# Performance work log

Measured on AMD Instinct MI355X. Metric: run time of the kernel, lower is better.

The kernel has to match this reference:

```python
import jax, jax.numpy as jnp
import numpy as np

LN_EPS = 1e-5


def setup_inputs() -> dict:
    key = jax.random.key(0)
    ks = jax.random.split(key, 10)
    N, E, D, H = 32000, 512000, 256, 128
    atom_features = jax.random.normal(ks[0], (N, D), dtype=jnp.float32)
    edge_features = jax.random.normal(ks[1], (E, H), dtype=jnp.float32)
    edge_index = jax.random.randint(ks[2], (2, E), 0, N, dtype=jnp.int64)
    s = lambda fan_in: 1.0 / np.sqrt(fan_in)
    W_lin = jax.random.normal(ks[3], (D, H), dtype=jnp.float32) * s(D)
    W1 = jax.random.normal(ks[4], (3 * H, H), dtype=jnp.float32) * s(3 * H)
    b1 = jnp.zeros((H,), jnp.float32)
    W2 = jax.random.normal(ks[5], (H, H), dtype=jnp.float32) * s(H)
    b2 = jnp.zeros((H,), jnp.float32)
    W3 = jax.random.normal(ks[6], (H, H), dtype=jnp.float32) * s(H)
    b3 = jnp.zeros((H,), jnp.float32)
    gamma = jnp.ones((H,), jnp.float32)
    beta = jnp.zeros((H,), jnp.float32)
    return dict(atom_features=atom_features, edge_features=edge_features,
                edge_index=edge_index, W_lin=W_lin, W1=W1, b1=b1, W2=W2,
                b2=b2, W3=W3, b3=b3, gamma=gamma, beta=beta)


def _layernorm(x, gamma, beta):
    mu = jnp.mean(x, axis=-1, keepdims=True)
    var = jnp.mean((x - mu) ** 2, axis=-1, keepdims=True)
    return (x - mu) * jax.lax.rsqrt(var + LN_EPS) * gamma + beta


def reference(atom_features, edge_features, edge_index, W_lin, W1, b1, W2, b2, W3, b3, gamma, beta):
    # o3.Linear on scalar irreps -> plain bias-free linear: [N, D] @ [D, H]
    atom_scalars = atom_features @ W_lin  # [N, H]
    edge_dst, edge_src = edge_index[0], edge_index[1]
    # gather + concat: [E, 3H]
    edge_in = jnp.concatenate(
        [atom_scalars[edge_dst], atom_scalars[edge_src], edge_features], axis=-1)
    h = jax.nn.relu(edge_in @ W1 + b1)
    h = jax.nn.relu(h @ W2 + b2)
    h = h @ W3 + b3  # [E, H]
    return _layernorm(edge_features + h, gamma, beta)
```

## Files before the change

### kernel.cpp

```cpp
#include <hip/hip_runtime.h>

typedef __attribute__((ext_vector_type(8))) short bf16x8;
typedef __attribute__((ext_vector_type(16))) float f32x16;
typedef __attribute__((ext_vector_type(4))) float f32x4;
typedef __attribute__((ext_vector_type(4))) unsigned u32x4;

#define LN_EPS 1e-5f

__device__ __forceinline__ unsigned short f2bf(float f) {
    unsigned u = __float_as_uint(f);
    unsigned r = (u + 0x7FFFu + ((u >> 16) & 1u)) >> 16;
    return (unsigned short)r;
}

__device__ __forceinline__ unsigned cvt_pk_bf16(float lo, float hi) {
    unsigned r;
    asm("v_cvt_pk_bf16_f32 %0, %1, %2" : "=v"(r) : "v"(lo), "v"(hi));
    return r;
}

__device__ __forceinline__ void permswap(unsigned& a, unsigned& b) {
    asm("v_permlane32_swap_b32 %0, %1" : "+v"(a), "+v"(b));
}

__global__ void prep_weights(const float* __restrict__ W_lin,
                             const float* __restrict__ W1,
                             const float* __restrict__ W2,
                             const float* __restrict__ W3,
                             unsigned short* __restrict__ wt_lin,
                             unsigned short* __restrict__ wimg) {
    int i = blockIdx.x * blockDim.x + threadIdx.x;
    if (i < 128 * 256) {
        int n = i >> 8, k = i & 255;
        wt_lin[n * 256 + k] = f2bf(W_lin[k * 128 + n]);
    } else if (i < 128 * 256 + 5 * 16384) {
        int j = i - 128 * 256;
        int mat = j >> 14, r = j & 16383;
        int jj = r & 7, l = (r >> 3) & 63, ks = (r >> 9) & 7, f = r >> 12;
        int n = 32 * f + (l & 31);
        int k = 16 * ks + 8 * (l >> 5) + jj;
        float v;
        if (mat < 3)       v = W1[(mat * 128 + k) * 128 + n];
        else if (mat == 3) v = W2[k * 128 + n];
        else               v = W3[k * 128 + n];
        wimg[j] = f2bf(v);
    }
}

__global__ void atoms_gemm(const float* __restrict__ af,
                           const unsigned short* __restrict__ wt_lin,
                           unsigned short* __restrict__ atoms_bf,
                           int Natoms) {
    const int wv = threadIdx.x >> 6, lane = threadIdx.x & 63;
    const int l31 = lane & 31, g8 = (lane >> 5) * 8, g4 = (lane >> 5) * 4;
    const int R = blockIdx.x * 128 + wv * 32;

    f32x16 acc[4];
#pragma unroll
    for (int f = 0; f < 4; ++f)
#pragma unroll
        for (int e = 0; e < 16; ++e) acc[f][e] = 0.0f;

    int arow = R + l31;
    if (arow >= Natoms) arow = Natoms - 1;
    const float* ap = af + (size_t)arow * 256;

#pragma unroll
    for (int ks = 0; ks < 16; ++ks) {
        const int k0 = ks * 16 + g8;
        float4 x0 = *(const float4*)(ap + k0);
        float4 x1 = *(const float4*)(ap + k0 + 4);
        bf16x8 a;
        a[0] = (short)f2bf(x0.x); a[1] = (short)f2bf(x0.y);
        a[2] = (short)f2bf(x0.z); a[3] = (short)f2bf(x0.w);
        a[4] = (short)f2bf(x1.x); a[5] = (short)f2bf(x1.y);
        a[6] = (short)f2bf(x1.z); a[7] = (short)f2bf(x1.w);
#pragma unroll
        for (int f = 0; f < 4; ++f) {
            bf16x8 b = *(const bf16x8*)(wt_lin + (32 * f + l31) * 256 + k0);
            acc[f] = __builtin_amdgcn_mfma_f32_32x32x16_bf16(a, b, acc[f], 0, 0, 0);
        }
    }

#pragma unroll
    for (int f = 0; f < 4; ++f) {
        const int col = 32 * f + l31;
#pragma unroll
        for (int r = 0; r < 16; ++r) {
            int row = R + (r & 3) + 8 * (r >> 2) + g4;
            if (row < Natoms) atoms_bf[(size_t)row * 128 + col] = f2bf(acc[f][r]);
        }
    }
}

__global__ __launch_bounds__(512, 2) void edge_fused(
    const float* __restrict__ ef, const int* __restrict__ eidx,
    const unsigned short* __restrict__ atoms_bf,
    const unsigned short* __restrict__ wimg,
    const float* __restrict__ b1, const float* __restrict__ b2,
    const float* __restrict__ b3, const float* __restrict__ gamma_,
    const float* __restrict__ beta_, float* __restrict__ out, int E) {
    __shared__ unsigned short wlds[2 * 16384];
    __shared__ unsigned short io[8][4096];

    const int tid = threadIdx.x;
    const int lane = tid & 63, wv = tid >> 6;
    const int l31 = lane & 31, hi = lane >> 5, h8 = hi * 8;

    {
        const char* s = (const char*)wimg;
        char* d = (char*)wlds;
        const int o = tid * 16;
#pragma unroll
        for (int i = 0; i < 8; ++i)
            __builtin_amdgcn_global_load_lds(
                (const __attribute__((address_space(1))) unsigned int*)(s + o + i * 8192),
                (__attribute__((address_space(3))) unsigned int*)(d + o + i * 8192),
                16, 0, 0);
    }

    const int edgeBase = blockIdx.x * 256 + wv * 32;
    const int e0 = edgeBase + l31;
    const int e = e0 < E ? e0 : E - 1;

    const int dI = eidx[e], sI = eidx[E + e];
    const unsigned short* dRow = atoms_bf + (size_t)dI * 128;
    const unsigned short* sRow = atoms_bf + (size_t)sI * 128;
    bf16x8 gd[8], gs[8];
#pragma unroll
    for (int ks = 0; ks < 8; ++ks) {
        gd[ks] = *(const bf16x8*)(dRow + ks * 16 + h8);
        gs[ks] = *(const bf16x8*)(sRow + ks * 16 + h8);
    }

    char* iow = (char*)&io[wv][0];
    {
        const int r4 = lane >> 4;
        const int c8 = (lane & 15) * 8;
#pragma unroll
        for (int i = 0; i < 8; ++i) {
            const int row = i * 4 + r4;
            int gr = edgeBase + row;
            if (gr >= E) gr = E - 1;
            const float* rp = ef + (size_t)gr * 128 + c8;
            f32x4 x0 = *(const f32x4*)(rp);
            f32x4 x1 = *(const f32x4*)(rp + 4);
            u32x4 w = (u32x4){cvt_pk_bf16(x0[0], x0[1]), cvt_pk_bf16(x0[2], x0[3]),
                              cvt_pk_bf16(x1[0], x1[1]), cvt_pk_bf16(x1[2], x1[3])};
            const int slot = (lane & 15) ^ (row & 7);
            *(u32x4*)(iow + row * 256 + slot * 16) = w;
        }
    }

#pragma unroll
    for (int ks = 0; ks < 8; ++ks)
        asm volatile("" :: "v"(gd[ks]), "v"(gs[ks]));

    f32x16 acc[4];
    auto initb = [&](const float* __restrict__ bb) {
#pragma unroll
        for (int f = 0; f < 4; ++f)
#pragma unroll
            for (int m = 0; m < 4; ++m) {
                f32x4 b4 = *(const f32x4*)(bb + 32 * f + 8 * m + 4 * hi);
#pragma unroll
                for (int i = 0; i < 4; ++i) acc[f][4 * m + i] = b4[i];
            }
    };

    bf16x8 frag[8];
    auto build_frags = [&]() {
#pragma unroll
        for (int f = 0; f < 4; ++f) {
            unsigned pk0[4], pk1[4];
#pragma unroll
            for (int m = 0; m < 4; ++m) {
                float a0 = fmaxf(acc[f][4 * m + 0], 0.0f);
                float a1 = fmaxf(acc[f][4 * m + 1], 0.0f);
                float a2 = fmaxf(acc[f][4 * m + 2], 0.0f);
                float a3 = fmaxf(acc[f][4 * m + 3], 0.0f);
                pk0[m] = cvt_pk_bf16(a0, a1);
                pk1[m] = cvt_pk_bf16(a2, a3);
            }
#pragma unroll
            for (int k1 = 0; k1 < 2; ++k1) {
                unsigned x0 = pk0[2 * k1], y0 = pk0[2 * k1 + 1];
                unsigned x1 = pk1[2 * k1], y1 = pk1[2 * k1 + 1];
                permswap(x0, y0);
                permswap(x1, y1);
                union { u32x4 u; bf16x8 b; } cv;
                cv.u = (u32x4){x0, x1, y0, y1};
                frag[2 * f + k1] = cv.b;
            }
        }
    };

    const unsigned short* lbase = wlds + lane * 8;
    const unsigned short* wg1c = wimg + 2 * 16384 + lane * 8;
    const unsigned short* wg2 = wimg + 3 * 16384 + lane * 8;
    const unsigned short* wg3 = wimg + 4 * 16384 + lane * 8;
    const int xr = l31 & 7;

    __syncthreads();

    initb(b1);
#pragma unroll
    for (int ks = 0; ks < 8; ++ks)
#pragma unroll
        for (int f = 0; f < 4; ++f) {
            bf16x8 a = *(const bf16x8*)(lbase + ((0 * 4 + f) * 8 + ks) * 512);
            acc[f] = __builtin_amdgcn_mfma_f32_32x32x16_bf16(a, gd[ks], acc[f], 0, 0, 0);
        }
#pragma unroll
    for (int ks = 0; ks < 8; ++ks)
#pragma unroll
        for (int f = 0; f < 4; ++f) {
            bf16x8 a = *(const bf16x8*)(lbase + ((1 * 4 + f) * 8 + ks) * 512);
            acc[f] = __builtin_amdgcn_mfma_f32_32x32x16_bf16(a, gs[ks], acc[f], 0, 0, 0);
        }
#pragma unroll
    for (int ks = 0; ks < 8; ++ks) {
        const int slot = (2 * ks + hi) ^ xr;
        bf16x8 bx = *(const bf16x8*)(iow + l31 * 256 + slot * 16);
#pragma unroll
        for (int f = 0; f < 4; ++f) {
            bf16x8 a = *(const bf16x8*)(wg1c + (f * 8 + ks) * 512);
            acc[f] = __builtin_amdgcn_mfma_f32_32x32x16_bf16(a, bx, acc[f], 0, 0, 0);
        }
    }

    build_frags();
    initb(b2);
#pragma unroll
    for (int ks = 0; ks < 8; ++ks)
#pragma unroll
        for (int f = 0; f < 4; ++f) {
            bf16x8 a = *(const bf16x8*)(wg2 + (f * 8 + ks) * 512);
            acc[f] = __builtin_amdgcn_mfma_f32_32x32x16_bf16(a, frag[ks], acc[f], 0, 0, 0);
        }

    build_frags();
    initb(b3);
#pragma unroll
    for (int ks = 0; ks < 8; ++ks)
#pragma unroll
        for (int f = 0; f < 4; ++f) {
            bf16x8 a = *(const bf16x8*)(wg3 + (f * 8 + ks) * 512);
            acc[f] = __builtin_amdgcn_mfma_f32_32x32x16_bf16(a, frag[ks], acc[f], 0, 0, 0);
        }

    float s = 0.0f, q = 0.0f;
#pragma unroll
    for (int f = 0; f < 4; ++f)
#pragma unroll
        for (int m = 0; m < 4; ++m) {
            const int slot = (4 * f + m) ^ xr;
            uint2 w = *(const uint2*)(iow + l31 * 256 + slot * 16 + 8 * hi);
            float r0 = __uint_as_float(w.x << 16);
            float r1 = __uint_as_float(w.x & 0xffff0000u);
            float r2 = __uint_as_float(w.y << 16);
            float r3 = __uint_as_float(w.y & 0xffff0000u);
            float v0 = acc[f][4 * m + 0] + r0;
            float v1 = acc[f][4 * m + 1] + r1;
            float v2 = acc[f][4 * m + 2] + r2;
            float v3 = acc[f][4 * m + 3] + r3;
            acc[f][4 * m + 0] = v0; acc[f][4 * m + 1] = v1;
            acc[f][4 * m + 2] = v2; acc[f][4 * m + 3] = v3;
            s += v0 + v1 + v2 + v3;
            q += v0 * v0 + v1 * v1 + v2 * v2 + v3 * v3;
        }
    s += __shfl_xor(s, 32, 64);
    q += __shfl_xor(q, 32, 64);
    const float mu = s * (1.0f / 128.0f);
    const float var = q * (1.0f / 128.0f) - mu * mu;
    const float rs = rsqrtf(var + LN_EPS);

#pragma unroll
    for (int h = 0; h < 2; ++h) {
#pragma unroll
        for (int f2 = 0; f2 < 2; ++f2) {
            const int f = 2 * h + f2;
#pragma unroll
            for (int m = 0; m < 4; ++m) {
                f32x4 g4 = *(const f32x4*)(gamma_ + 32 * f + 8 * m + 4 * hi);
                f32x4 be4 = *(const f32x4*)(beta_ + 32 * f + 8 * m + 4 * hi);
                f32x4 o;
#pragma unroll
                for (int i = 0; i < 4; ++i)
                    o[i] = (acc[f][4 * m + i] - mu) * rs * g4[i] + be4[i];
                const int slot = (8 * f2 + 2 * m + hi) ^ xr;
                *(f32x4*)(iow + l31 * 256 + slot * 16) = o;
            }
        }
        const int r4 = lane >> 4;
#pragma unroll
        for (int i = 0; i < 8; ++i) {
            const int row = i * 4 + r4;
            const int slot = (lane & 15) ^ (row & 7);
            f32x4 v = *(const f32x4*)(iow + row * 256 + slot * 16);
            const int edge = edgeBase + row;
            if (edge < E)
                *(f32x4*)(out + (size_t)edge * 128 + h * 64 + (lane & 15) * 4) = v;
        }
    }
}

extern "C" void kernel_launch(void* const* d_in, const int* in_sizes, int n_in,
                              void* d_out, int out_size, void* d_ws, size_t ws_size,
                              hipStream_t stream) {
    const float* atom_features = (const float*)d_in[0];
    const float* edge_features = (const float*)d_in[1];
    const int* edge_index = (const int*)d_in[2];
    const float* W_lin = (const float*)d_in[3];
    const float* W1 = (const float*)d_in[4];
    const float* b1 = (const float*)d_in[5];
    const float* W2 = (const float*)d_in[6];
    const float* b2 = (const float*)d_in[7];
    const float* W3 = (const float*)d_in[8];
    const float* b3 = (const float*)d_in[9];
    const float* gamma_ = (const float*)d_in[10];
    const float* beta_ = (const float*)d_in[11];
    float* out = (float*)d_out;

    const int Natoms = in_sizes[0] / 256;
    const int E = in_sizes[1] / 128;

    unsigned short* atoms_bf = (unsigned short*)d_ws;
    unsigned short* wt_lin = atoms_bf + (size_t)Natoms * 128;
    unsigned short* wimg = wt_lin + 128 * 256;

    const int prep_items = 128 * 256 + 5 * 16384;
    prep_weights<<<(prep_items + 255) / 256, 256, 0, stream>>>(W_lin, W1, W2, W3,
                                                               wt_lin, wimg);
    atoms_gemm<<<(Natoms + 127) / 128, 256, 0, stream>>>(atom_features, wt_lin,
                                                         atoms_bf, Natoms);
    edge_fused<<<(E + 255) / 256, 512, 0, stream>>>(edge_features, edge_index,
                                                    atoms_bf, wimg, b1, b2, b3,
                                                    gamma_, beta_, out, E);
}
```

Before: 253.9 us.

## Process two 32-edge tiles per wave to amortize weight LDS load

Each wave now handles two 32-edge tiles sequentially, and the grid is halved. Gather loads for both tiles are issued up front, and the first-layer weight image copied into LDS is reused across twice as many edges. This is meant to amortize the per-block weight staging and hide gather latency for the second tile behind the first tile's MFMA work. The cost is higher register pressure from holding 32 extra bf16x8 gather fragments, which may lower occupancy, and the second tile's edge-feature fill is serialized after the first tile.

```diff
diff --git a/kernel.cpp b/kernel.cpp
--- a/kernel.cpp
+++ b/kernel.cpp
@@ -119,28 +119,38 @@
                 16, 0, 0);
     }
 
-    const int edgeBase = blockIdx.x * 256 + wv * 32;
-    const int e0 = edgeBase + l31;
-    const int e = e0 < E ? e0 : E - 1;
-
-    const int dI = eidx[e], sI = eidx[E + e];
-    const unsigned short* dRow = atoms_bf + (size_t)dI * 128;
-    const unsigned short* sRow = atoms_bf + (size_t)sI * 128;
-    bf16x8 gd[8], gs[8];
+    const int baseA = blockIdx.x * 512 + wv * 64;
+    const int baseB = baseA + 32;
+    const int eA = (baseA + l31) < E ? (baseA + l31) : E - 1;
+    const int eB = (baseB + l31) < E ? (baseB + l31) : E - 1;
+
+    const int dIA = eidx[eA], sIA = eidx[E + eA];
+    const int dIB = eidx[eB], sIB = eidx[E + eB];
+    const unsigned short* dRowA = atoms_bf + (size_t)dIA * 128;
+    const unsigned short* sRowA = atoms_bf + (size_t)sIA * 128;
+    const unsigned short* dRowB = atoms_bf + (size_t)dIB * 128;
+    const unsigned short* sRowB = atoms_bf + (size_t)sIB * 128;
+
+    bf16x8 gdA[8], gsA[8], gdB[8], gsB[8];
 #pragma unroll
     for (int ks = 0; ks < 8; ++ks) {
-        gd[ks] = *(const bf16x8*)(dRow + ks * 16 + h8);
-        gs[ks] = *(const bf16x8*)(sRow + ks * 16 + h8);
-    }
+        gdA[ks] = *(const bf16x8*)(dRowA + ks * 16 + h8);
+        gsA[ks] = *(const bf16x8*)(sRowA + ks * 16 + h8);
+        gdB[ks] = *(const bf16x8*)(dRowB + ks * 16 + h8);
+        gsB[ks] = *(const bf16x8*)(sRowB + ks * 16 + h8);
+    }
+#pragma unroll
+    for (int ks = 0; ks < 8; ++ks)
+        asm volatile("" :: "v"(gdA[ks]), "v"(gsA[ks]), "v"(gdB[ks]), "v"(gsB[ks]));
 
     char* iow = (char*)&io[wv][0];
-    {
-        const int r4 = lane >> 4;
-        const int c8 = (lane & 15) * 8;
+    const int r4 = lane >> 4;
+    const int c8 = (lane & 15) * 8;
+    auto fill_ef = [&](int base) {
 #pragma unroll
         for (int i = 0; i < 8; ++i) {
             const int row = i * 4 + r4;
-            int gr = edgeBase + row;
+            int gr = base + row;
             if (gr >= E) gr = E - 1;
             const float* rp = ef + (size_t)gr * 128 + c8;
             f32x4 x0 = *(const f32x4*)(rp);
@@ -150,14 +160,16 @@
             const int slot = (lane & 15) ^ (row & 7);
             *(u32x4*)(iow + row * 256 + slot * 16) = w;
         }
-    }
-
-#pragma unroll
-    for (int ks = 0; ks < 8; ++ks)
-        asm volatile("" :: "v"(gd[ks]), "v"(gs[ks]));
-
-    f32x16 acc[4];
-    auto initb = [&](const float* __restrict__ bb) {
+    };
+    fill_ef(baseA);
+
+    const unsigned short* lbase = wlds + lane * 8;
+    const unsigned short* wg1c = wimg + 2 * 16384 + lane * 8;
+    const unsigned short* wg2 = wimg + 3 * 16384 + lane * 8;
+    const unsigned short* wg3 = wimg + 4 * 16384 + lane * 8;
+    const int xr = l31 & 7;
+
+    auto initb = [&](f32x16* acc, const float* __restrict__ bb) {
 #pragma unroll
         for (int f = 0; f < 4; ++f)
 #pragma unroll
@@ -168,8 +180,7 @@
             }
     };
 
-    bf16x8 frag[8];
-    auto build_frags = [&]() {
+    auto build_frags = [&](f32x16* acc, bf16x8* frag) {
 #pragma unroll
         for (int f = 0; f < 4; ++f) {
             unsigned pk0[4], pk1[4];
@@ -195,114 +206,113 @@
         }
     };
 
-    const unsigned short* lbase = wlds + lane * 8;
-    const unsigned short* wg1c = wimg + 2 * 16384 + lane * 8;
-    const unsigned short* wg2 = wimg + 3 * 16384 + lane * 8;
-    const unsigned short* wg3 = wimg + 4 * 16384 + lane * 8;
-    const int xr = l31 & 7;
+    auto compute_tile = [&](int base, bf16x8* gd, bf16x8* gs) {
+        f32x16 acc[4];
+        bf16x8 frag[8];
+        initb(acc, b1);
+#pragma unroll
+        for (int ks = 0; ks < 8; ++ks)
+#pragma unroll
+            for (int f = 0; f < 4; ++f) {
+                bf16x8 a = *(const bf16x8*)(lbase + ((0 * 4 + f) * 8 + ks) * 512);
+                acc[f] = __builtin_amdgcn_mfma_f32_32x32x16_bf16(a, gd[ks], acc[f], 0, 0, 0);
+            }
+#pragma unroll
+        for (int ks = 0; ks < 8; ++ks)
+#pragma unroll
+            for (int f = 0; f < 4; ++f) {
+                bf16x8 a = *(const bf16x8*)(lbase + ((1 * 4 + f) * 8 + ks) * 512);
+                acc[f] = __builtin_amdgcn_mfma_f32_32x32x16_bf16(a, gs[ks], acc[f], 0, 0, 0);
+            }
+#pragma unroll
+        for (int ks = 0; ks < 8; ++ks) {
+            const int slot = (2 * ks + hi) ^ xr;
+            bf16x8 bx = *(const bf16x8*)(iow + l31 * 256 + slot * 16);
+#pragma unroll
+            for (int f = 0; f < 4; ++f) {
+                bf16x8 a = *(const bf16x8*)(wg1c + (f * 8 + ks) * 512);
+                acc[f] = __builtin_amdgcn_mfma_f32_32x32x16_bf16(a, bx, acc[f], 0, 0, 0);
+            }
+        }
+        build_frags(acc, frag);
+        initb(acc, b2);
+#pragma unroll
+        for (int ks = 0; ks < 8; ++ks)
+#pragma unroll
+            for (int f = 0; f < 4; ++f) {
+                bf16x8 a = *(const bf16x8*)(wg2 + (f * 8 + ks) * 512);
+                acc[f] = __builtin_amdgcn_mfma_f32_32x32x16_bf16(a, frag[ks], acc[f], 0, 0, 0);
+            }
+        build_frags(acc, frag);
+        initb(acc, b3);
+#pragma unroll
+        for (int ks = 0; ks < 8; ++ks)
+#pragma unroll
+            for (int f = 0; f < 4; ++f) {
+                bf16x8 a = *(const bf16x8*)(wg3 + (f * 8 + ks) * 512);
+                acc[f] = __builtin_amdgcn_mfma_f32_32x32x16_bf16(a, frag[ks], acc[f], 0, 0, 0);
+            }
+        float s = 0.0f, q = 0.0f;
+#pragma unroll
+        for (int f = 0; f < 4; ++f)
+#pragma unroll
+            for (int m = 0; m < 4; ++m) {
+                const int slot = (4 * f + m) ^ xr;
+                uint2 w = *(const uint2*)(iow + l31 * 256 + slot * 16 + 8 * hi);
+                float r0 = __uint_as_float(w.x << 16);
+                float r1 = __uint_as_float(w.x & 0xffff0000u);
+                float r2 = __uint_as_float(w.y << 16);
+                float r3 = __uint_as_float(w.y & 0xffff0000u);
+                float v0 = acc[f][4 * m + 0] + r0;
+                float v1 = acc[f][4 * m + 1] + r1;
+                float v2 = acc[f][4 * m + 2] + r2;
+                float v3 = acc[f][4 * m + 3] + r3;
+                acc[f][4 * m + 0] = v0; acc[f][4 * m + 1] = v1;
+                acc[f][4 * m + 2] = v2; acc[f][4 * m + 3] = v3;
+                s += v0 + v1 + v2 + v3;
+                q += v0 * v0 + v1 * v1 + v2 * v2 + v3 * v3;
+            }
+        s += __shfl_xor(s, 32, 64);
+        q += __shfl_xor(q, 32, 64);
+        const float mu = s * (1.0f / 128.0f);
+        const float var = q * (1.0f / 128.0f) - mu * mu;
+        const float rs = rsqrtf(var + LN_EPS);
+
+#pragma unroll
+        for (int h = 0; h < 2; ++h) {
+#pragma unroll
+            for (int f2 = 0; f2 < 2; ++f2) {
+                const int f = 2 * h + f2;
+#pragma unroll
+                for (int m = 0; m < 4; ++m) {
+                    f32x4 g4 = *(const f32x4*)(gamma_ + 32 * f + 8 * m + 4 * hi);
+                    f32x4 be4 = *(const f32x4*)(beta_ + 32 * f + 8 * m + 4 * hi);
+                    f32x4 o;
+#pragma unroll
+                    for (int i = 0; i < 4; ++i)
+                        o[i] = (acc[f][4 * m + i] - mu) * rs * g4[i] + be4[i];
+                    const int slot = (8 * f2 + 2 * m + hi) ^ xr;
+                    *(f32x4*)(iow + l31 * 256 + slot * 16) = o;
+                }
+            }
+#pragma unroll
+            for (int i = 0; i < 8; ++i) {
+                const int row = i * 4 + r4;
+                const int slot = (lane & 15) ^ (row & 7);
+                f32x4 v = *(const f32x4*)(iow + row * 256 + slot * 16);
+                const int edge = base + row;
+                if (edge < E)
+                    *(f32x4*)(out + (size_t)edge * 128 + h * 64 + (lane & 15) * 4) = v;
+            }
+        }
+    };
 
     __syncthreads();
 
-    initb(b1);
-#pragma unroll
-    for (int ks = 0; ks < 8; ++ks)
-#pragma unroll
-        for (int f = 0; f < 4; ++f) {
-            bf16x8 a = *(const bf16x8*)(lbase + ((0 * 4 + f) * 8 + ks) * 512);
-            acc[f] = __builtin_amdgcn_mfma_f32_32x32x16_bf16(a, gd[ks], acc[f], 0, 0, 0);
-        }
-#pragma unroll
-    for (int ks = 0; ks < 8; ++ks)
-#pragma unroll
-        for (int f = 0; f < 4; ++f) {
-            bf16x8 a = *(const bf16x8*)(lbase + ((1 * 4 + f) * 8 + ks) * 512);
-            acc[f] = __builtin_amdgcn_mfma_f32_32x32x16_bf16(a, gs[ks], acc[f], 0, 0, 0);
-        }
-#pragma unroll
-    for (int ks = 0; ks < 8; ++ks) {
-        const int slot = (2 * ks + hi) ^ xr;
-        bf16x8 bx = *(const bf16x8*)(iow + l31 * 256 + slot * 16);
-#pragma unroll
-        for (int f = 0; f < 4; ++f) {
-            bf16x8 a = *(const bf16x8*)(wg1c + (f * 8 + ks) * 512);
-            acc[f] = __builtin_amdgcn_mfma_f32_32x32x16_bf16(a, bx, acc[f], 0, 0, 0);
-        }
-    }
-
-    build_frags();
-    initb(b2);
-#pragma unroll
-    for (int ks = 0; ks < 8; ++ks)
-#pragma unroll
-        for (int f = 0; f < 4; ++f) {
-            bf16x8 a = *(const bf16x8*)(wg2 + (f * 8 + ks) * 512);
-            acc[f] = __builtin_amdgcn_mfma_f32_32x32x16_bf16(a, frag[ks], acc[f], 0, 0, 0);
-        }
-
-    build_frags();
-    initb(b3);
-#pragma unroll
-    for (int ks = 0; ks < 8; ++ks)
-#pragma unroll
-        for (int f = 0; f < 4; ++f) {
-            bf16x8 a = *(const bf16x8*)(wg3 + (f * 8 + ks) * 512);
-            acc[f] = __builtin_amdgcn_mfma_f32_32x32x16_bf16(a, frag[ks], acc[f], 0, 0, 0);
-        }
-
-    float s = 0.0f, q = 0.0f;
-#pragma unroll
-    for (int f = 0; f < 4; ++f)
-#pragma unroll
-        for (int m = 0; m < 4; ++m) {
-            const int slot = (4 * f + m) ^ xr;
-            uint2 w = *(const uint2*)(iow + l31 * 256 + slot * 16 + 8 * hi);
-            float r0 = __uint_as_float(w.x << 16);
-            float r1 = __uint_as_float(w.x & 0xffff0000u);
-            float r2 = __uint_as_float(w.y << 16);
-            float r3 = __uint_as_float(w.y & 0xffff0000u);
-            float v0 = acc[f][4 * m + 0] + r0;
-            float v1 = acc[f][4 * m + 1] + r1;
-            float v2 = acc[f][4 * m + 2] + r2;
-            float v3 = acc[f][4 * m + 3] + r3;
-            acc[f][4 * m + 0] = v0; acc[f][4 * m + 1] = v1;
-            acc[f][4 * m + 2] = v2; acc[f][4 * m + 3] = v3;
-            s += v0 + v1 + v2 + v3;
-            q += v0 * v0 + v1 * v1 + v2 * v2 + v3 * v3;
-        }
-    s += __shfl_xor(s, 32, 64);
-    q += __shfl_xor(q, 32, 64);
-    const float mu = s * (1.0f / 128.0f);
-    const float var = q * (1.0f / 128.0f) - mu * mu;
-    const float rs = rsqrtf(var + LN_EPS);
-
-#pragma unroll
-    for (int h = 0; h < 2; ++h) {
-#pragma unroll
-        for (int f2 = 0; f2 < 2; ++f2) {
-            const int f = 2 * h + f2;
-#pragma unroll
-            for (int m = 0; m < 4; ++m) {
-                f32x4 g4 = *(const f32x4*)(gamma_ + 32 * f + 8 * m + 4 * hi);
-                f32x4 be4 = *(const f32x4*)(beta_ + 32 * f + 8 * m + 4 * hi);
-                f32x4 o;
-#pragma unroll
-                for (int i = 0; i < 4; ++i)
-                    o[i] = (acc[f][4 * m + i] - mu) * rs * g4[i] + be4[i];
-                const int slot = (8 * f2 + 2 * m + hi) ^ xr;
-                *(f32x4*)(iow + l31 * 256 + slot * 16) = o;
-            }
-        }
-        const int r4 = lane >> 4;
-#pragma unroll
-        for (int i = 0; i < 8; ++i) {
-            const int row = i * 4 + r4;
-            const int slot = (lane & 15) ^ (row & 7);
-            f32x4 v = *(const f32x4*)(iow + row * 256 + slot * 16);
-            const int edge = edgeBase + row;
-            if (edge < E)
-                *(f32x4*)(out + (size_t)edge * 128 + h * 64 + (lane & 15) * 4) = v;
-        }
-    }
+    compute_tile(baseA, gdA, gsA);
+
+    fill_ef(baseB);
+    compute_tile(baseB, gdB, gsB);
 }
 
 extern "C" void kernel_launch(void* const* d_in, const int* in_sizes, int n_in,
@@ -334,7 +344,7 @@
                                                                wt_lin, wimg);
     atoms_gemm<<<(Natoms + 127) / 128, 256, 0, stream>>>(atom_features, wt_lin,
                                                          atoms_bf, Natoms);
-    edge_fused<<<(E + 255) / 256, 512, 0, stream>>>(edge_features, edge_index,
+    edge_fused<<<(E + 511) / 512, 512, 0, stream>>>(edge_features, edge_index,
                                                     atoms_bf, wimg, b1, b2, b3,
                                                     gamma_, beta_, out, E);
 }
```

Result: slower. 439.8 us (+73.2%).
